# Kernel tuning notes

Measured on AMD Instinct MI355X. Metric: run time of the kernel, lower is better.

## Reference

```python
import math
import jax, jax.numpy as jnp
import numpy as np

B, T = 4, 512
STATE_DIM, ACT_DIM = 17, 18
H, NH, L, MAXT = 1024, 16, 4, 4096
S = 3 * T          # interleaved (rtg, state, action) sequence length
D = H // NH
FF = 4 * H
LN_EPS = 1e-5


def setup_inputs() -> dict:
    key = jax.random.key(0)
    ks = jax.random.split(key, 32)
    init = lambda k, shape: jax.random.normal(k, shape, jnp.float32) * 0.02
    inp = {
        "states": jax.random.normal(ks[0], (B, T, STATE_DIM), jnp.float32),
        "returns_to_go": jax.random.normal(ks[1], (B, T, 1), jnp.float32),
        "timesteps": jax.random.randint(ks[2], (B, T), 0, MAXT),
        "actions": jax.random.randint(ks[3], (B, T), 0, ACT_DIM),
        "bandera": 0,
        # embeddings / input projections
        "embed_time_table": init(ks[4], (MAXT, H)),
        "embed_act_table": init(ks[5], (ACT_DIM, H)),
        "Wrtg": init(ks[6], (1, H)), "brtg": jnp.zeros((H,), jnp.float32),
        "Wst": init(ks[7], (STATE_DIM, H)), "bst": jnp.zeros((H,), jnp.float32),
        # per-block params, stacked over L layers
        "Wq": init(ks[8], (L, H, H)), "bq": jnp.zeros((L, H), jnp.float32),
        "Wk": init(ks[9], (L, H, H)), "bk": jnp.zeros((L, H), jnp.float32),
        "Wv": init(ks[10], (L, H, H)), "bv": jnp.zeros((L, H), jnp.float32),
        "Wo": init(ks[11], (L, H, H)), "bo": jnp.zeros((L, H), jnp.float32),
        "W1": init(ks[12], (L, H, FF)), "b1": jnp.zeros((L, FF), jnp.float32),
        "W2": init(ks[13], (L, FF, H)), "b2": jnp.zeros((L, H), jnp.float32),
        # prediction heads
        "Wpr": init(ks[14], (H, 1)), "bpr": jnp.zeros((1,), jnp.float32),
        "Wps": init(ks[15], (H, STATE_DIM)), "bps": jnp.zeros((STATE_DIM,), jnp.float32),
        "Wpa": init(ks[16], (H, ACT_DIM)), "bpa": jnp.zeros((ACT_DIM,), jnp.float32),
    }
    return inp


def _ln(x):
    # LayerNorm, elementwise_affine=False
    m = jnp.mean(x, axis=-1, keepdims=True)
    v = jnp.mean((x - m) ** 2, axis=-1, keepdims=True)
    return (x - m) * jax.lax.rsqrt(v + LN_EPS)


def reference(states, returns_to_go, embed_time_table, embed_act_table,
              Wrtg, brtg, Wst, bst,
              Wq, bq, Wk, bk, Wv, bv, Wo, bo,
              W1, b1, W2, b2,
              Wpr, bpr, Wps, bps, Wpa, bpa,
              timesteps, actions, bandera):
    te = embed_time_table[timesteps]                      # [B,T,H]
    r = returns_to_go @ Wrtg + brtg + te                  # [B,T,H]
    s = states @ Wst + bst + te                           # [B,T,H]
    a = embed_act_table[actions] + te                     # [B,T,H]
    # interleave (r_t, s_t, a_t) along time -> [B, 3T, H]
    h = jnp.stack([r, s, a], axis=2).reshape(B, S, H)
    h = _ln(h)
    mask = jnp.tril(jnp.ones((S, S), bool))
    scale = 1.0 / math.sqrt(D)
    for i in range(L):
        q = (h @ Wq[i] + bq[i]).reshape(B, S, NH, D).transpose(0, 2, 1, 3)
        k = (h @ Wk[i] + bk[i]).reshape(B, S, NH, D).transpose(0, 2, 1, 3)
        v = (h @ Wv[i] + bv[i]).reshape(B, S, NH, D).transpose(0, 2, 1, 3)
        sc = jnp.einsum('bhqd,bhkd->bhqk', q, k) * scale  # [B,NH,S,S]
        sc = jnp.where(mask, sc, -jnp.inf)
        att = jax.nn.softmax(sc, axis=-1)
        o = jnp.einsum('bhqk,bhkd->bhqd', att, v)
        o = o.transpose(0, 2, 1, 3).reshape(B, S, H)
        h = _ln(h + o @ Wo[i] + bo[i])
        m = jax.nn.gelu(h @ W1[i] + b1[i], approximate=False) @ W2[i] + b2[i]
        h = _ln(h + m)
    hh = h.reshape(B, T, 3, H)
    h_s = hh[:, :, 1]   # token after (..., r_t, s_t)
    h_a = hh[:, :, 2]   # token after (..., r_t, s_t, a_t)
    return_preds = h_a @ Wpr + bpr                        # [B,T,1]
    state_preds = h_a @ Wps + bps                         # [B,T,STATE_DIM]
    action_preds = h_s @ Wpa + bpa                        # [B,T,ACT_DIM]
    return (state_preds, action_preds, return_preds)
```

## Files before the change

### kernel.cpp

```cpp
#include <hip/hip_runtime.h>
#include <hip/hip_bf16.h>
#include <math.h>

#define Bc 4
#define Tc 512
#define Sc 1536
#define Hc 1024
#define NHc 16
#define Dc 64
#define FFc 4096
#define Lc 4
#define Mrows (Bc*Tc*3)
#define LN_EPS 1e-5f

typedef __attribute__((ext_vector_type(4))) float  f32x4;
typedef __attribute__((ext_vector_type(8))) short  s16x8;
typedef __attribute__((ext_vector_type(4))) short  s16x4;

__device__ __forceinline__ short f2b(float f) {
    union { __hip_bfloat16 h; short s; } u;
    u.h = __float2bfloat16(f);
    return u.s;
}

__device__ __forceinline__ void gload16(const void* g, void* l) {
    __builtin_amdgcn_global_load_lds(
        (const __attribute__((address_space(1))) void*)g,
        (__attribute__((address_space(3))) void*)l, 16, 0, 0);
}

__global__ __launch_bounds__(256) void embed_kernel(
    const float* __restrict__ states, const float* __restrict__ rtg,
    const int* __restrict__ timesteps, const int* __restrict__ actions,
    const float* __restrict__ ett, const float* __restrict__ eat,
    const float* __restrict__ Wrtg, const float* __restrict__ brtg,
    const float* __restrict__ Wst, const float* __restrict__ bst,
    float* __restrict__ h)
{
    const int bt = blockIdx.x;
    const int b = bt / Tc, t = bt % Tc;
    const int ts = timesteps[bt];
    const int ac = actions[bt];
    const float rv = rtg[bt];
    const float* te = ett + (size_t)ts * Hc;
    const float* ea = eat + (size_t)ac * Hc;
    __shared__ float sst[17];
    if (threadIdx.x < 17) sst[threadIdx.x] = states[bt * 17 + threadIdx.x];
    __syncthreads();
    float* hr = h + ((size_t)b * Sc + 3 * t) * Hc;
    for (int j = threadIdx.x; j < Hc; j += 256) {
        const float tej = te[j];
        hr[j] = rv * Wrtg[j] + brtg[j] + tej;
        float sv = bst[j];
        #pragma unroll
        for (int qx = 0; qx < 17; ++qx) sv += sst[qx] * Wst[qx * Hc + j];
        hr[Hc + j] = sv + tej;
        hr[2 * Hc + j] = ea[j] + tej;
    }
}

__global__ __launch_bounds__(256) void resln_kernel(float* __restrict__ h,
                                                    const float* __restrict__ add,
                                                    short* __restrict__ hb)
{
    const size_t row = blockIdx.x;
    float4* hr = reinterpret_cast<float4*>(h + row * Hc);
    const int tid = threadIdx.x;
    float4 x = hr[tid];
    if (add != nullptr) {
        const float4 a = reinterpret_cast<const float4*>(add + row * Hc)[tid];
        x.x += a.x; x.y += a.y; x.z += a.z; x.w += a.w;
    }
    float s1 = x.x + x.y + x.z + x.w;
    float s2 = x.x*x.x + x.y*x.y + x.z*x.z + x.w*x.w;
    #pragma unroll
    for (int off = 32; off > 0; off >>= 1) {
        s1 += __shfl_xor(s1, off);
        s2 += __shfl_xor(s2, off);
    }
    __shared__ float r1[4], r2[4];
    const int wv = tid >> 6, lane = tid & 63;
    if (lane == 0) { r1[wv] = s1; r2[wv] = s2; }
    __syncthreads();
    s1 = r1[0] + r1[1] + r1[2] + r1[3];
    s2 = r2[0] + r2[1] + r2[2] + r2[3];
    const float mean = s1 * (1.0f / Hc);
    const float var  = s2 * (1.0f / Hc) - mean * mean;
    const float rs = rsqrtf(var + LN_EPS);
    x.x = (x.x - mean) * rs; x.y = (x.y - mean) * rs;
    x.z = (x.z - mean) * rs; x.w = (x.w - mean) * rs;
    hr[tid] = x;
    if (hb != nullptr) {
        s16x4 o; o[0] = f2b(x.x); o[1] = f2b(x.y); o[2] = f2b(x.z); o[3] = f2b(x.w);
        *(s16x4*)&hb[row * Hc + tid * 4] = o;
    }
}

__global__ __launch_bounds__(256) void wconv_all_kernel(
    const float* __restrict__ Wq, const float* __restrict__ Wk,
    const float* __restrict__ Wv, const float* __restrict__ Wo,
    const float* __restrict__ W1, const float* __restrict__ W2,
    short* __restrict__ wqkv_t, short* __restrict__ wo_t,
    short* __restrict__ w1_t, short* __restrict__ w2_t)
{
    __shared__ float Ls[64][68];
    const int blk = blockIdx.x;
    const float* src; short* dst; int N, dstStride, dstRow0, tx, ty;
    if (blk < 1024) {
        const int m = blk >> 8;
        const int local = blk & 255;
        tx = local & 15; ty = local >> 4;
        N = 1024; dstStride = 1024;
        if (m == 0)      { src = Wq; dst = wqkv_t; dstRow0 = 0; }
        else if (m == 1) { src = Wk; dst = wqkv_t; dstRow0 = 1024; }
        else if (m == 2) { src = Wv; dst = wqkv_t; dstRow0 = 2048; }
        else             { src = Wo; dst = wo_t;   dstRow0 = 0; }
    } else if (blk < 2048) {
        const int local = blk - 1024;
        tx = local & 63; ty = local >> 6;
        src = W1; dst = w1_t; N = 4096; dstStride = 1024; dstRow0 = 0;
    } else {
        const int local = blk - 2048;
        tx = local & 15; ty = local >> 4;
        src = W2; dst = w2_t; N = 1024; dstStride = 4096; dstRow0 = 0;
    }
    const int n0 = tx * 64, k0 = ty * 64;
    const int tid = threadIdx.x;
    #pragma unroll
    for (int it = 0; it < 4; ++it) {
        const int idx = tid + 256 * it;
        const int r = idx >> 4, c4 = idx & 15;
        *(f32x4*)&Ls[r][c4 * 4] = *(const f32x4*)(src + (size_t)(k0 + r) * N + n0 + c4 * 4);
    }
    __syncthreads();
    #pragma unroll
    for (int it = 0; it < 2; ++it) {
        const int idx = tid + 256 * it;
        const int n = idx & 63, k8 = idx >> 6;
        s16x8 o;
        #pragma unroll
        for (int j = 0; j < 8; ++j) o[j] = f2b(Ls[k8 * 8 + j][n]);
        *(s16x8*)(dst + (size_t)(dstRow0 + n0 + n) * dstStride + k0 + k8 * 8) = o;
    }
}

__global__ __launch_bounds__(256) void biaspack_kernel(
    const float* __restrict__ bq, const float* __restrict__ bk,
    const float* __restrict__ bv, float* __restrict__ pb)
{
    const int idx = blockIdx.x * 256 + threadIdx.x;
    const int l = idx / 3072, j = idx % 3072;
    float v;
    if (j < 1024) v = bq[l * 1024 + j];
    else if (j < 2048) v = bk[l * 1024 + j - 1024];
    else v = bv[l * 1024 + j - 2048];
    pb[idx] = v;
}

__global__ __launch_bounds__(256) void headspack_kernel(
    const float* __restrict__ Wps, const float* __restrict__ bps,
    const float* __restrict__ Wpr, const float* __restrict__ bpr,
    const float* __restrict__ Wpa, const float* __restrict__ bpa,
    short* __restrict__ Wha, short* __restrict__ Whb,
    float* __restrict__ biasA, float* __restrict__ biasB)
{
    const int n = blockIdx.x & 63, set = blockIdx.x >> 6;
    const int tid = threadIdx.x;
    if (tid == 0) {
        if (set == 0) biasA[n] = (n < 17) ? bps[n] : (n == 17 ? bpr[0] : 0.f);
        else          biasB[n] = (n < 18) ? bpa[n] : 0.f;
    }
    short* dst = (set == 0 ? Wha : Whb) + (size_t)n * 1024;
    for (int k = tid; k < 1024; k += 256) {
        float v;
        if (set == 0) v = (n < 17) ? Wps[(size_t)k * 17 + n] : (n == 17 ? Wpr[k] : 0.f);
        else          v = (n < 18) ? Wpa[(size_t)k * 18 + n] : 0.f;
        dst[k] = f2b(v);
    }
}

__global__ __launch_bounds__(256) void headsgather_kernel(
    const float* __restrict__ scrA, const float* __restrict__ scrB,
    float* __restrict__ out)
{
    const int idx = blockIdx.x * 256 + threadIdx.x;
    if (idx >= 2048 * 36) return;
    const int bt = idx / 36, j = idx % 36;
    if (j < 17)      out[bt * 17 + j] = scrA[bt * 64 + j];
    else if (j < 35) out[2048 * 17 + bt * 18 + (j - 17)] = scrB[bt * 64 + (j - 17)];
    else             out[2048 * 35 + bt] = scrA[bt * 64 + 17];
}

template<int BN, int DO_GELU, int OUTBF16>
__global__ __launch_bounds__(256) void gemm_bb(
    const short* __restrict__ A, const short* __restrict__ Bt,
    const float* __restrict__ bias, void* __restrict__ Cv,
    int M, int N, int K, int arm, int aro)
{
    constexpr int NJ = BN / 32;
    __shared__ short As[2 * 128 * 32];
    __shared__ short Bs[2 * BN * 32];
    const int tid = threadIdx.x, lane = tid & 63, wid = tid >> 6;
    const int wr = wid >> 1, wc = wid & 1;
    const int g = lane >> 4, ql = lane & 15;
    const int m0 = blockIdx.y * 128, n0 = blockIdx.x * BN;

    const int crow = lane >> 2;
    const int csw  = ((lane & 3) ^ ((crow >> 1) & 3)) * 8;

    const short* Ag0 = A + ((size_t)arm * (m0 + wid * 32 + crow) + aro) * K + csw;
    const short* Ag1 = A + ((size_t)arm * (m0 + wid * 32 + 16 + crow) + aro) * K + csw;
    const int a0off = (wid * 32) * 32;
    const int a1off = (wid * 32 + 16) * 32;

    const short* Bg0; const short* Bg1 = nullptr;
    int b0off = 0, b1off = 0;
    if constexpr (BN == 128) {
        Bg0 = Bt + (size_t)(n0 + wid * 32 + crow) * K + csw;
        Bg1 = Bt + (size_t)(n0 + wid * 32 + 16 + crow) * K + csw;
        b0off = (wid * 32) * 32;
        b1off = (wid * 32 + 16) * 32;
    } else {
        Bg0 = Bt + (size_t)(n0 + wid * 16 + crow) * K + csw;
        b0off = (wid * 16) * 32;
    }

    auto stage = [&](int buf, int k0) {
        short* Ab = &As[buf * (128 * 32)];
        short* Bb = &Bs[buf * (BN * 32)];
        gload16(Ag0 + k0, Ab + a0off);
        gload16(Ag1 + k0, Ab + a1off);
        gload16(Bg0 + k0, Bb + b0off);
        if constexpr (BN == 128) gload16(Bg1 + k0, Bb + b1off);
    };

    const int rslot = (g ^ ((ql >> 1) & 3)) * 8;
    const int aoffr = (wr * 64 + ql) * 32 + rslot;
    const int boffr = (wc * (BN / 2) + ql) * 32 + rslot;

    f32x4 acc[4][NJ] = {};
    stage(0, 0);
    stage(1, 32);
    int cur = 0;
    for (int k0 = 0; k0 < K; k0 += 32) {
        if (k0 + 32 < K) {
            if constexpr (BN == 128) asm volatile("s_waitcnt vmcnt(4)" ::: "memory");
            else                     asm volatile("s_waitcnt vmcnt(3)" ::: "memory");
        } else {
            asm volatile("s_waitcnt vmcnt(0)" ::: "memory");
        }
        __builtin_amdgcn_s_barrier();

        const short* Acur = &As[cur * (128 * 32)];
        const short* Bcur = &Bs[cur * (BN * 32)];
        s16x8 af[4], bfr[NJ];
        #pragma unroll
        for (int mi = 0; mi < 4; ++mi)
            af[mi] = *(const s16x8*)&Acur[aoffr + mi * (16 * 32)];
        #pragma unroll
        for (int nj = 0; nj < NJ; ++nj)
            bfr[nj] = *(const s16x8*)&Bcur[boffr + nj * (16 * 32)];

        asm volatile("s_waitcnt lgkmcnt(0)" ::: "memory");
        __builtin_amdgcn_sched_barrier(0);
        __builtin_amdgcn_s_barrier();

        if (k0 + 64 < K) stage(cur, k0 + 64);

        #pragma unroll
        for (int mi = 0; mi < 4; ++mi)
            #pragma unroll
            for (int nj = 0; nj < NJ; ++nj)
                acc[mi][nj] = __builtin_amdgcn_mfma_f32_16x16x32_bf16(
                    af[mi], bfr[nj], acc[mi][nj], 0, 0, 0);
        cur ^= 1;
    }

    #pragma unroll
    for (int mi = 0; mi < 4; ++mi) {
        #pragma unroll
        for (int nj = 0; nj < NJ; ++nj) {
            const int col = n0 + wc * (BN / 2) + nj * 16 + ql;
            const float bv = bias[col];
            #pragma unroll
            for (int r = 0; r < 4; ++r) {
                const int row = m0 + wr * 64 + mi * 16 + g * 4 + r;
                float v = acc[mi][nj][r] + bv;
                if constexpr (DO_GELU)
                    v = 0.5f * v * (1.0f + erff(v * 0.70710678118654752f));
                if constexpr (OUTBF16)
                    ((short*)Cv)[(size_t)row * N + col] = f2b(v);
                else
                    ((float*)Cv)[(size_t)row * N + col] = v;
            }
        }
    }
}

__global__ __launch_bounds__(256) void vtrans_kernel(
    const short* __restrict__ v, int vs, short* __restrict__ vt)
{
    const int nkt = Sc / 64;
    const int blk = blockIdx.x;
    const int bh = blk / nkt, kt = blk % nkt;
    const int b = bh / NHc, hh = bh % NHc;
    __shared__ short Ls[64][64];
    const int tid = threadIdx.x;
    #pragma unroll
    for (int i = 0; i < 2; ++i) {
        const int idx = tid + 256 * i;
        const int r = idx >> 3, c8 = idx & 7;
        const int cs = c8 ^ (r & 7) ^ (r >> 3);
        *(s16x8*)&Ls[r][cs * 8] =
            *(const s16x8*)(v + ((size_t)(b * Sc + kt * 64 + r)) * vs + hh * 64 + c8 * 8);
    }
    __syncthreads();
    #pragma unroll
    for (int i = 0; i < 2; ++i) {
        const int idx = tid + 256 * i;
        const int d = idx >> 3, k8 = idx & 7;
        s16x8 o;
        #pragma unroll
        for (int j = 0; j < 8; ++j) {
            const int kv = k8 * 8 + j;
            const int cs = (d >> 3) ^ (kv & 7) ^ (kv >> 3);
            o[j] = Ls[kv][cs * 8 + (d & 7)];
        }
        *(s16x8*)(vt + ((size_t)bh * 64 + d) * Sc + kt * 64 + k8 * 8) = o;
    }
}

__global__ __launch_bounds__(256) void attn_kernel(
    const short* __restrict__ qg, const short* __restrict__ kg,
    const short* __restrict__ vtg, short* __restrict__ og, int qks)
{
    const int nqt = Sc / 64;
    const int blk = blockIdx.x;
    const int bh = blk / nqt;
    const int qt = (nqt - 1) - (blk % nqt);
    const int b = bh / NHc, hh = bh % NHc;
    const int tid = threadIdx.x, lane = tid & 63, w = tid >> 6;
    const int g = lane >> 4, ql = lane & 15;

    __shared__ short Ks[2][64 * 64];
    __shared__ short Vs[2][64 * 64];
    __shared__ short Qs[64][72];
    __shared__ short Ps[4][16][72];

    const size_t baseq = ((size_t)b * Sc) * qks + hh * Dc;

    #pragma unroll
    for (int i = 0; i < 2; ++i) {
        const int idx = tid + 256 * i;
        const int r = idx >> 3, c8 = idx & 7;
        *(s16x8*)&Qs[r][c8 * 8] =
            *(const s16x8*)(qg + baseq + (size_t)(qt * 64 + r) * qks + c8 * 8);
    }
    __syncthreads();
    const s16x8 bq0 = *(const s16x8*)&Qs[w * 16 + ql][g * 8];
    const s16x8 bq1 = *(const s16x8*)&Qs[w * 16 + ql][32 + g * 8];

    const int srow = lane >> 3;
    const int r0 = w * 8 + srow;
    const int r1 = 32 + w * 8 + srow;
    const int g0 = ((lane & 7) ^ (r0 & 7)) * 8;
    const int g1 = ((lane & 7) ^ (r1 & 7)) * 8;
    const short* kg0 = kg + baseq + (size_t)r0 * qks + g0;
    const short* kg1 = kg + baseq + (size_t)r1 * qks + g1;
    const short* vg0 = vtg + ((size_t)bh * 64 + r0) * Sc + g0;
    const short* vg1 = vtg + ((size_t)bh * 64 + r1) * Sc + g1;

    auto stageKV = [&](int buf, int kt) {
        const size_t ko = (size_t)kt * 64 * qks;
        const size_t vo = (size_t)kt * 64;
        gload16(kg0 + ko, &Ks[buf][w * 512]);
        gload16(kg1 + ko, &Ks[buf][2048 + w * 512]);
        gload16(vg0 + vo, &Vs[buf][w * 512]);
        gload16(vg1 + vo, &Vs[buf][2048 + w * 512]);
    };

    const int kx = ql & 7;
    const int gr0 = (g ^ kx) * 8;
    const int gr1 = ((4 + g) ^ kx) * 8;

    f32x4 acc_o[4] = {};
    float m = -1e30f, l = 0.f;
    const int qrow = qt * 64 + w * 16 + ql;

    stageKV(0, 0);
    for (int kt = 0; kt <= qt; ++kt) {
        const int buf = kt & 1;
        if (kt < qt) {
            stageKV(buf ^ 1, kt + 1);
            asm volatile("s_waitcnt vmcnt(4)" ::: "memory");
        } else {
            asm volatile("s_waitcnt vmcnt(0)" ::: "memory");
        }
        __builtin_amdgcn_s_barrier();

        s16x8 ka0[4], ka1[4], vv0[4], vv1[4];
        #pragma unroll
        for (int mi = 0; mi < 4; ++mi) {
            ka0[mi] = *(const s16x8*)&Ks[buf][(mi * 16 + ql) * 64 + gr0];
            ka1[mi] = *(const s16x8*)&Ks[buf][(mi * 16 + ql) * 64 + gr1];
            vv0[mi] = *(const s16x8*)&Vs[buf][(mi * 16 + ql) * 64 + gr0];
            vv1[mi] = *(const s16x8*)&Vs[buf][(mi * 16 + ql) * 64 + gr1];
        }
        asm volatile("s_waitcnt lgkmcnt(0)" ::: "memory");
        __builtin_amdgcn_sched_barrier(0);
        __builtin_amdgcn_s_barrier();

        f32x4 sacc[4] = {};
        #pragma unroll
        for (int mi = 0; mi < 4; ++mi) {
            sacc[mi] = __builtin_amdgcn_mfma_f32_16x16x32_bf16(ka0[mi], bq0, sacc[mi], 0, 0, 0);
            sacc[mi] = __builtin_amdgcn_mfma_f32_16x16x32_bf16(ka1[mi], bq1, sacc[mi], 0, 0, 0);
        }

        float pv[16];
        float pm = -1e30f;
        #pragma unroll
        for (int mi = 0; mi < 4; ++mi)
            #pragma unroll
            for (int r = 0; r < 4; ++r) {
                const int kv = kt * 64 + mi * 16 + g * 4 + r;
                const float s = (kv <= qrow) ? sacc[mi][r] * 0.125f : -1e30f;
                pv[mi * 4 + r] = s;
                pm = fmaxf(pm, s);
            }
        pm = fmaxf(pm, __shfl_xor(pm, 16));
        pm = fmaxf(pm, __shfl_xor(pm, 32));
        const float m2 = fmaxf(m, pm);
        const float corr = __expf(m - m2);
        m = m2;
        float ps = 0.f;
        #pragma unroll
        for (int i = 0; i < 16; ++i) { pv[i] = __expf(pv[i] - m2); ps += pv[i]; }
        ps += __shfl_xor(ps, 16);
        ps += __shfl_xor(ps, 32);
        l = l * corr + ps;

        #pragma unroll
        for (int mi = 0; mi < 4; ++mi) {
            s16x4 pw;
            #pragma unroll
            for (int r = 0; r < 4; ++r) pw[r] = f2b(pv[mi * 4 + r]);
            *(s16x4*)&Ps[w][ql][mi * 16 + g * 4] = pw;
        }

        float corr_r[4];
        #pragma unroll
        for (int r = 0; r < 4; ++r) corr_r[r] = __shfl(corr, g * 4 + r);
        #pragma unroll
        for (int nj = 0; nj < 4; ++nj)
            #pragma unroll
            for (int r = 0; r < 4; ++r) acc_o[nj][r] *= corr_r[r];

        const s16x8 pa0 = *(const s16x8*)&Ps[w][ql][g * 8];
        const s16x8 pa1 = *(const s16x8*)&Ps[w][ql][32 + g * 8];
        #pragma unroll
        for (int nj = 0; nj < 4; ++nj) {
            acc_o[nj] = __builtin_amdgcn_mfma_f32_16x16x32_bf16(pa0, vv0[nj], acc_o[nj], 0, 0, 0);
            acc_o[nj] = __builtin_amdgcn_mfma_f32_16x16x32_bf16(pa1, vv1[nj], acc_o[nj], 0, 0, 0);
        }
    }

    const float rl = 1.0f / l;
    float rl_r[4];
    #pragma unroll
    for (int r = 0; r < 4; ++r) rl_r[r] = __shfl(rl, g * 4 + r);
    const size_t baseo = ((size_t)b * Sc) * Hc + hh * Dc;
    #pragma unroll
    for (int nj = 0; nj < 4; ++nj)
        #pragma unroll
        for (int r = 0; r < 4; ++r) {
            const int qr = qt * 64 + w * 16 + g * 4 + r;
            og[baseo + (size_t)qr * Hc + nj * 16 + ql] = f2b(acc_o[nj][r] * rl_r[r]);
        }
}

extern "C" void kernel_launch(void* const* d_in, const int* in_sizes, int n_in,
                              void* d_out, int out_size, void* d_ws, size_t ws_size,
                              hipStream_t stream)
{
    const float* states = (const float*)d_in[0];
    const float* rtg    = (const float*)d_in[1];
    const int*   timesteps = (const int*)d_in[2];
    const int*   actions   = (const int*)d_in[3];
    const float* ett  = (const float*)d_in[5];
    const float* eat  = (const float*)d_in[6];
    const float* Wrtg = (const float*)d_in[7];
    const float* brtg = (const float*)d_in[8];
    const float* Wst  = (const float*)d_in[9];
    const float* bst  = (const float*)d_in[10];
    const float* Wq = (const float*)d_in[11];
    const float* bq = (const float*)d_in[12];
    const float* Wk = (const float*)d_in[13];
    const float* bk = (const float*)d_in[14];
    const float* Wv = (const float*)d_in[15];
    const float* bv = (const float*)d_in[16];
    const float* Wo = (const float*)d_in[17];
    const float* bo = (const float*)d_in[18];
    const float* W1 = (const float*)d_in[19];
    const float* b1 = (const float*)d_in[20];
    const float* W2 = (const float*)d_in[21];
    const float* b2 = (const float*)d_in[22];
    const float* Wpr = (const float*)d_in[23];
    const float* bpr = (const float*)d_in[24];
    const float* Wps = (const float*)d_in[25];
    const float* bps = (const float*)d_in[26];
    const float* Wpa = (const float*)d_in[27];
    const float* bpa = (const float*)d_in[28];
    float* out = (float*)d_out;

    char* wsb = (char*)d_ws;
    const size_t MH = (size_t)Mrows * Hc;
    const int nAttnBlk = Bc * NHc * (Sc / 64);

    const size_t off_h    = 0;
    const size_t off_hb   = off_h    + MH * 4;
    const size_t off_qkv  = off_hb   + MH * 2;
    const size_t off_vt   = off_qkv  + MH * 6;
    const size_t off_ob   = off_vt   + MH * 2;
    const size_t off_rb   = off_ob   + MH * 2;
    const size_t off_wl   = off_rb   + MH * 4;
    const size_t wl_qkv   = 0;
    const size_t wl_wo    = wl_qkv + (size_t)3072 * 1024 * 2;
    const size_t wl_w1    = wl_wo  + (size_t)1024 * 1024 * 2;
    const size_t wl_w2    = wl_w1  + (size_t)4096 * 1024 * 2;
    const size_t wl_bytes = wl_w2  + (size_t)1024 * 4096 * 2;
    const size_t off_pb   = off_wl + wl_bytes;
    const size_t NEED     = off_pb + (size_t)Lc * 3072 * 4;
    (void)NEED;

    float* h   = (float*)(wsb + off_h);
    short* hb  = (short*)(wsb + off_hb);
    short* qkv = (short*)(wsb + off_qkv);
    short* vt  = (short*)(wsb + off_vt);
    short* ob  = (short*)(wsb + off_ob);
    float* rb  = (float*)(wsb + off_rb);
    short* gb  = qkv;
    short* wqkv_t = (short*)(wsb + off_wl + wl_qkv);
    short* wo_t   = (short*)(wsb + off_wl + wl_wo);
    short* w1_t   = (short*)(wsb + off_wl + wl_w1);
    short* w2_t   = (short*)(wsb + off_wl + wl_w2);
    float* pb     = (float*)(wsb + off_pb);
    short* Wha   = vt;
    short* Whb   = vt + 64 * 1024;
    float* biasA = (float*)(vt + 2 * 64 * 1024);
    float* biasB = biasA + 64;
    float* scrA  = rb;
    float* scrB  = rb + 2048 * 64;

    biaspack_kernel<<<Lc * 12, 256, 0, stream>>>(bq, bk, bv, pb);
    embed_kernel<<<Bc * Tc, 256, 0, stream>>>(states, rtg, timesteps, actions,
                                              ett, eat, Wrtg, brtg, Wst, bst, h);
    resln_kernel<<<Mrows, 256, 0, stream>>>(h, nullptr, hb);

    const dim3 gQKV(3072 / 128, Mrows / 128);
    const dim3 gFF1(FFc / 128, Mrows / 128);
    const dim3 gN1K(1024 / 128, Mrows / 128);

    for (int i = 0; i < Lc; ++i) {
        const size_t wofH = (size_t)i * Hc * Hc;
        const size_t wofF = (size_t)i * Hc * FFc;
        wconv_all_kernel<<<3072, 256, 0, stream>>>(
            Wq + wofH, Wk + wofH, Wv + wofH, Wo + wofH, W1 + wofF, W2 + wofF,
            wqkv_t, wo_t, w1_t, w2_t);

        gemm_bb<128,0,1><<<gQKV, 256, 0, stream>>>(hb, wqkv_t, pb + i * 3072, qkv, Mrows, 3072, 1024, 1, 0);
        vtrans_kernel<<<nAttnBlk, 256, 0, stream>>>(qkv + 2048, 3072, vt);
        attn_kernel<<<nAttnBlk, 256, 0, stream>>>(qkv, qkv + 1024, vt, ob, 3072);
        gemm_bb<128,0,0><<<gN1K, 256, 0, stream>>>(ob, wo_t, bo + i * Hc, rb, Mrows, 1024, 1024, 1, 0);
        resln_kernel<<<Mrows, 256, 0, stream>>>(h, rb, hb);

        gemm_bb<128,1,1><<<gFF1, 256, 0, stream>>>(hb, w1_t, b1 + i * FFc, gb, Mrows, 4096, 1024, 1, 0);
        gemm_bb<128,0,0><<<gN1K, 256, 0, stream>>>(gb, w2_t, b2 + i * Hc, rb, Mrows, 1024, 4096, 1, 0);
        resln_kernel<<<Mrows, 256, 0, stream>>>(h, rb, hb);
    }

    headspack_kernel<<<128, 256, 0, stream>>>(Wps, bps, Wpr, bpr, Wpa, bpa,
                                              Wha, Whb, biasA, biasB);
    gemm_bb<64,0,0><<<dim3(1, 16), 256, 0, stream>>>(hb, Wha, biasA, scrA, 2048, 64, 1024, 3, 2);
    gemm_bb<64,0,0><<<dim3(1, 16), 256, 0, stream>>>(hb, Whb, biasB, scrB, 2048, 64, 1024, 3, 1);
    headsgather_kernel<<<288, 256, 0, stream>>>(scrA, scrB, out);
}
```

Measured before the change: 1.513 ms.

## Use 128x256 GEMM tiles for QKV/FF1 and fuse V transpose into QKV epilogue

Adds a wider-tile GEMM kernel (128x256 block, 4x8 MFMA tiles per wave) for the QKV and FF1 projections, raising arithmetic intensity per loaded tile. The QKV epilogue writes the V section directly in transposed per-head layout, which removes the separate vtrans kernel and its extra read/write pass over V. Head weights are moved to the ob buffer because vt is now written during the QKV GEMM. In exchange, the wider tiles use more registers (128 accumulator floats per thread) and halve the number of blocks, which may reduce occupancy. The transposed stores are scattered 8-byte writes.

```diff
diff --git a/kernel.cpp b/kernel.cpp
--- a/kernel.cpp
+++ b/kernel.cpp
@@ -191,6 +191,114 @@
     else             out[2048 * 35 + bt] = scrA[bt * 64 + 17];
 }
 
+template<int DO_GELU, int OUTBF16, int VT_FUSE>
+__global__ __launch_bounds__(256) void gemm_bw(
+    const short* __restrict__ A, const short* __restrict__ Bt,
+    const float* __restrict__ bias, void* __restrict__ Cv,
+    int M, int N, int K, short* __restrict__ vt)
+{
+    __shared__ short As[2 * 128 * 32];
+    __shared__ short Bs[2 * 256 * 32];
+    const int tid = threadIdx.x, lane = tid & 63, wid = tid >> 6;
+    const int wr = (wid >> 1) & 1, wc = wid & 1;
+    const int g = lane >> 4, ql = lane & 15;
+    const int m0 = blockIdx.y * 128, n0 = blockIdx.x * 256;
+
+    const short* ag[2]; const short* bg[4];
+    #pragma unroll
+    for (int i = 0; i < 2; ++i) {
+        const int ci = tid + 256 * i, r = ci >> 2, sl = (ci & 3) ^ ((r >> 1) & 3);
+        ag[i] = A + (size_t)(m0 + r) * K + sl * 8;
+    }
+    #pragma unroll
+    for (int i = 0; i < 4; ++i) {
+        const int ci = tid + 256 * i, r = ci >> 2, sl = (ci & 3) ^ ((r >> 1) & 3);
+        bg[i] = Bt + (size_t)(n0 + r) * K + sl * 8;
+    }
+
+    auto stage = [&](int buf, int k0) {
+        #pragma unroll
+        for (int i = 0; i < 2; ++i)
+            gload16(ag[i] + k0, &As[buf * 4096 + (tid + 256 * i) * 8]);
+        #pragma unroll
+        for (int i = 0; i < 4; ++i)
+            gload16(bg[i] + k0, &Bs[buf * 8192 + (tid + 256 * i) * 8]);
+    };
+
+    const int rx = (ql >> 1) & 3;
+    const int aoffr = (wr * 64 + ql) * 32 + (g ^ rx) * 8;
+    const int boffr = (wc * 128 + ql) * 32 + (g ^ rx) * 8;
+
+    f32x4 acc[4][8] = {};
+    stage(0, 0);
+    stage(1, 32);
+    int cur = 0;
+    for (int k0 = 0; k0 < K; k0 += 32) {
+        if (k0 + 32 < K) asm volatile("s_waitcnt vmcnt(6)" ::: "memory");
+        else             asm volatile("s_waitcnt vmcnt(0)" ::: "memory");
+        __builtin_amdgcn_s_barrier();
+
+        const short* Acur = &As[cur * 4096];
+        const short* Bcur = &Bs[cur * 8192];
+        s16x8 af[4], bfr[8];
+        #pragma unroll
+        for (int mi = 0; mi < 4; ++mi)
+            af[mi] = *(const s16x8*)&Acur[aoffr + mi * 512];
+        #pragma unroll
+        for (int nj = 0; nj < 8; ++nj)
+            bfr[nj] = *(const s16x8*)&Bcur[boffr + nj * 512];
+
+        asm volatile("s_waitcnt lgkmcnt(0)" ::: "memory");
+        __builtin_amdgcn_sched_barrier(0);
+        __builtin_amdgcn_s_barrier();
+
+        if (k0 + 64 < K) stage(cur, k0 + 64);
+
+        #pragma unroll
+        for (int mi = 0; mi < 4; ++mi)
+            #pragma unroll
+            for (int nj = 0; nj < 8; ++nj)
+                acc[mi][nj] = __builtin_amdgcn_mfma_f32_16x16x32_bf16(
+                    af[mi], bfr[nj], acc[mi][nj], 0, 0, 0);
+        cur ^= 1;
+    }
+
+    #pragma unroll
+    for (int mi = 0; mi < 4; ++mi) {
+        #pragma unroll
+        for (int nj = 0; nj < 8; ++nj) {
+            const int col = n0 + wc * 128 + nj * 16 + ql;
+            const float bv = bias[col];
+            float vals[4];
+            #pragma unroll
+            for (int r = 0; r < 4; ++r) {
+                float v = acc[mi][nj][r] + bv;
+                if constexpr (DO_GELU)
+                    v = 0.5f * v * (1.0f + erff(v * 0.70710678118654752f));
+                vals[r] = v;
+            }
+            if (VT_FUSE && col >= 2048) {
+                const int row0 = m0 + wr * 64 + mi * 16 + g * 4;
+                const int b = row0 / Sc, s = row0 % Sc;
+                const int cc = col - 2048, hh = cc >> 6, d = cc & 63;
+                s16x4 o;
+                #pragma unroll
+                for (int r = 0; r < 4; ++r) o[r] = f2b(vals[r]);
+                *(s16x4*)(vt + (((size_t)(b * NHc + hh) * 64 + d) * Sc + s)) = o;
+            } else {
+                #pragma unroll
+                for (int r = 0; r < 4; ++r) {
+                    const int row = m0 + wr * 64 + mi * 16 + g * 4 + r;
+                    if constexpr (OUTBF16)
+                        ((short*)Cv)[(size_t)row * N + col] = f2b(vals[r]);
+                    else
+                        ((float*)Cv)[(size_t)row * N + col] = vals[r];
+                }
+            }
+        }
+    }
+}
+
 template<int BN, int DO_GELU, int OUTBF16>
 __global__ __launch_bounds__(256) void gemm_bb(
     const short* __restrict__ A, const short* __restrict__ Bt,
@@ -294,39 +402,6 @@
                     ((float*)Cv)[(size_t)row * N + col] = v;
             }
         }
-    }
-}
-
-__global__ __launch_bounds__(256) void vtrans_kernel(
-    const short* __restrict__ v, int vs, short* __restrict__ vt)
-{
-    const int nkt = Sc / 64;
-    const int blk = blockIdx.x;
-    const int bh = blk / nkt, kt = blk % nkt;
-    const int b = bh / NHc, hh = bh % NHc;
-    __shared__ short Ls[64][64];
-    const int tid = threadIdx.x;
-    #pragma unroll
-    for (int i = 0; i < 2; ++i) {
-        const int idx = tid + 256 * i;
-        const int r = idx >> 3, c8 = idx & 7;
-        const int cs = c8 ^ (r & 7) ^ (r >> 3);
-        *(s16x8*)&Ls[r][cs * 8] =
-            *(const s16x8*)(v + ((size_t)(b * Sc + kt * 64 + r)) * vs + hh * 64 + c8 * 8);
-    }
-    __syncthreads();
-    #pragma unroll
-    for (int i = 0; i < 2; ++i) {
-        const int idx = tid + 256 * i;
-        const int d = idx >> 3, k8 = idx & 7;
-        s16x8 o;
-        #pragma unroll
-        for (int j = 0; j < 8; ++j) {
-            const int kv = k8 * 8 + j;
-            const int cs = (d >> 3) ^ (kv & 7) ^ (kv >> 3);
-            o[j] = Ls[kv][cs * 8 + (d & 7)];
-        }
-        *(s16x8*)(vt + ((size_t)bh * 64 + d) * Sc + kt * 64 + k8 * 8) = o;
     }
 }
 
@@ -530,8 +605,6 @@
     const size_t wl_w2    = wl_w1  + (size_t)4096 * 1024 * 2;
     const size_t wl_bytes = wl_w2  + (size_t)1024 * 4096 * 2;
     const size_t off_pb   = off_wl + wl_bytes;
-    const size_t NEED     = off_pb + (size_t)Lc * 3072 * 4;
-    (void)NEED;
 
     float* h   = (float*)(wsb + off_h);
     short* hb  = (short*)(wsb + off_hb);
@@ -545,9 +618,9 @@
     short* w1_t   = (short*)(wsb + off_wl + wl_w1);
     short* w2_t   = (short*)(wsb + off_wl + wl_w2);
     float* pb     = (float*)(wsb + off_pb);
-    short* Wha   = vt;
-    short* Whb   = vt + 64 * 1024;
-    float* biasA = (float*)(vt + 2 * 64 * 1024);
+    short* Wha   = ob;
+    short* Whb   = ob + 64 * 1024;
+    float* biasA = (float*)(ob + 2 * 64 * 1024);
     float* biasB = biasA + 64;
     float* scrA  = rb;
     float* scrB  = rb + 2048 * 64;
@@ -557,8 +630,8 @@
                                               ett, eat, Wrtg, brtg, Wst, bst, h);
     resln_kernel<<<Mrows, 256, 0, stream>>>(h, nullptr, hb);
 
-    const dim3 gQKV(3072 / 128, Mrows / 128);
-    const dim3 gFF1(FFc / 128, Mrows / 128);
+    const dim3 gQKV(3072 / 256, Mrows / 128);
+    const dim3 gFF1(FFc / 256, Mrows / 128);
     const dim3 gN1K(1024 / 128, Mrows / 128);
 
     for (int i = 0; i < Lc; ++i) {
@@ -568,13 +641,12 @@
             Wq + wofH, Wk + wofH, Wv + wofH, Wo + wofH, W1 + wofF, W2 + wofF,
             wqkv_t, wo_t, w1_t, w2_t);
 
-        gemm_bb<128,0,1><<<gQKV, 256, 0, stream>>>(hb, wqkv_t, pb + i * 3072, qkv, Mrows, 3072, 1024, 1, 0);
-        vtrans_kernel<<<nAttnBlk, 256, 0, stream>>>(qkv + 2048, 3072, vt);
+        gemm_bw<0,1,1><<<gQKV, 256, 0, stream>>>(hb, wqkv_t, pb + i * 3072, qkv, Mrows, 3072, 1024, vt);
         attn_kernel<<<nAttnBlk, 256, 0, stream>>>(qkv, qkv + 1024, vt, ob, 3072);
         gemm_bb<128,0,0><<<gN1K, 256, 0, stream>>>(ob, wo_t, bo + i * Hc, rb, Mrows, 1024, 1024, 1, 0);
         resln_kernel<<<Mrows, 256, 0, stream>>>(h, rb, hb);
 
-        gemm_bb<128,1,1><<<gFF1, 256, 0, stream>>>(hb, w1_t, b1 + i * FFc, gb, Mrows, 4096, 1024, 1, 0);
+        gemm_bw<1,1,0><<<gFF1, 256, 0, stream>>>(hb, w1_t, b1 + i * FFc, gb, Mrows, 4096, 1024, nullptr);
         gemm_bb<128,0,0><<<gN1K, 256, 0, stream>>>(gb, w2_t, b2 + i * Hc, rb, Mrows, 1024, 4096, 1, 0);
         resln_kernel<<<Mrows, 256, 0, stream>>>(h, rb, hb);
     }
```

After: 1.967 ms. +30.0%, slower.
